# Kernel tuning notes

Hardware: AMD Instinct MI355X
Metric: run time of the kernel (lower is better)

The kernel has to match this reference:

```python
import jax, jax.numpy as jnp
import numpy as np


def setup_inputs() -> dict:
    key = jax.random.key(0)
    k1, k2 = jax.random.split(key)
    B, N, D = 16, 2048, 256      # batch, tokens, token_dim
    C, K = 8, 1024               # num_codebooks, num_tokens
    x_in = jax.random.normal(k1, (B, N, D), dtype=jnp.float32)
    # torch.rand init for each VQCodebook embedding -> uniform[0,1)
    codebooks = jax.random.uniform(k2, (C, K, D), dtype=jnp.float32)
    return {"x_in": x_in, "codebooks": codebooks}


def _apply_one_codebook(x_res, emb, code_sg):
    d2 = (
        jnp.sum(x_res * x_res, axis=-1, keepdims=True)
        - 2.0 * jnp.einsum("bnd,kd->bnk", x_res, emb)
        + jnp.sum(emb * emb, axis=-1)
    )
    idx = jnp.argmin(d2, axis=-1)          # (B,N)
    z_q = emb[idx]                         # (B,N,D) gather
    if code_sg:                            # straight-through estimator
        z_q = x_res + jax.lax.stop_gradient(z_q - x_res)
    return z_q, idx


def reference(x_in, codebooks, code_sg=True):
    C = codebooks.shape[0]
    x_res = x_in
    z_q = jnp.zeros_like(x_in)
    idx_list = []
    for i in range(C):  # sequential residual dependency, loop over fixed num_codebooks
        # faithful to original: subtracts CUMULATIVE z_q each iteration
        x_res = x_res - z_q
        z_q_i, idx_i = _apply_one_codebook(x_res, codebooks[i], code_sg)
        z_q = z_q + z_q_i
        idx_list.append(idx_i)
    indices = jnp.stack(idx_list, axis=-2)  # (B, C, N)
    return z_q, indices
```

## Files before the change

### kernel.cpp

```cpp
#include <hip/hip_runtime.h>

#define TOKENS   32768
#define DIM      256
#define KCB      1024
#define CBOOKS   8
#define NTOK     2048
#define ZQ_ELEMS (TOKENS * DIM)
#define EPS_GAP  2.0e-2f

typedef _Float16 f16x8 __attribute__((ext_vector_type(8)));
typedef float    f32x4 __attribute__((ext_vector_type(4)));

__device__ float np_pairwise_sumsq_256(const float4* a4) {
  #pragma clang fp contract(off)
  float h[2];
  for (int hh = 0; hh < 2; ++hh) {
    const float4* b = a4 + hh * 32;
    float4 v0 = b[0], v1 = b[1];
    float r0 = v0.x * v0.x, r1 = v0.y * v0.y, r2 = v0.z * v0.z, r3 = v0.w * v0.w;
    float r4 = v1.x * v1.x, r5 = v1.y * v1.y, r6 = v1.z * v1.z, r7 = v1.w * v1.w;
    for (int t = 1; t < 16; ++t) {
      float4 w0 = b[2 * t], w1 = b[2 * t + 1];
      r0 = r0 + w0.x * w0.x; r1 = r1 + w0.y * w0.y;
      r2 = r2 + w0.z * w0.z; r3 = r3 + w0.w * w0.w;
      r4 = r4 + w1.x * w1.x; r5 = r5 + w1.y * w1.y;
      r6 = r6 + w1.z * w1.z; r7 = r7 + w1.w * w1.w;
    }
    h[hh] = ((r0 + r1) + (r2 + r3)) + ((r4 + r5) + (r6 + r7));
  }
  return h[0] + h[1];
}

__device__ __forceinline__ float4 f4_muladd(float4 a, float4 b, float4 c) {
  #pragma clang fp contract(off)
  float4 r;
  r.x = a.x * b.x + c.x;
  r.y = a.y * b.y + c.y;
  r.z = a.z * b.z + c.z;
  r.w = a.w * b.w + c.w;
  return r;
}

__global__ __launch_bounds__(256) void rvq_norms_kernel(
    const float* __restrict__ cb, float* __restrict__ sume) {
  int row = blockIdx.x * 256 + threadIdx.x;
  sume[row] = np_pairwise_sumsq_256((const float4*)&cb[(size_t)row * DIM]);
}

__global__ __launch_bounds__(256) void rvq_efsplit_kernel(
    const float* __restrict__ cbc, f16x8* __restrict__ EfC) {
  int gw = blockIdx.x * 4 + (threadIdx.x >> 6);
  int l  = threadIdx.x & 63;
  int row = gw * 16 + (l & 15);
  #pragma unroll
  for (int kb = 0; kb < 8; ++kb) {
    int d0 = kb * 32 + ((l >> 4) << 3);
    float4 u = *(const float4*)&cbc[(size_t)row * DIM + d0];
    float4 v = *(const float4*)&cbc[(size_t)row * DIM + d0 + 4];
    float ev[8] = {u.x, u.y, u.z, u.w, v.x, v.y, v.z, v.w};
    f16x8 hi, lo;
    #pragma unroll
    for (int i = 0; i < 8; ++i) {
      _Float16 h = (_Float16)ev[i];
      hi[i] = h; lo[i] = (_Float16)(ev[i] - (float)h);
    }
    EfC[((size_t)gw * 16 + kb) * 64 + l]     = hi;
    EfC[((size_t)gw * 16 + kb + 8) * 64 + l] = lo;
  }
}

__global__ __launch_bounds__(256) void rvq_screen_kernel(
    const float* __restrict__ xr, const f16x8* __restrict__ EfC,
    const float* __restrict__ sume, float4* __restrict__ part,
    int* __restrict__ fix_cnt) {
  __shared__ f16x8 ldsA[2][8][64];

  const int tid  = threadIdx.x;
  const int lane = tid & 63;
  const int wid  = tid >> 6;
  const int wm   = wid & 1;
  const int wn   = wid >> 1;
  const int mtile = blockIdx.x & 255;
  const int ntile = blockIdx.x >> 8;
  const int m0  = mtile * 128;

  if (blockIdx.x == 0 && tid == 0) *fix_cnt = 0;

  const f16x8* EfW = EfC + ((size_t)(ntile * 8 + wn * 4) * 16) * 64 + lane;

  f32x4 acc[4][4];
  #pragma unroll
  for (int mi = 0; mi < 4; ++mi)
    #pragma unroll
    for (int ni = 0; ni < 4; ++ni) acc[mi][ni] = (f32x4){0.f, 0.f, 0.f, 0.f};

  float4 ga[2][2];

#define LOADG(KC_)                                                           \
  { _Pragma("unroll")                                                        \
    for (int j = 0; j < 2; ++j) {                                            \
      int item = j * 256 + tid;                                              \
      int row = item >> 2, q8 = item & 3;                                    \
      const float* sa = &xr[(size_t)(m0 + row) * DIM + (KC_) * 32 + q8 * 8]; \
      ga[j][0] = *(const float4*)sa; ga[j][1] = *(const float4*)(sa + 4);    \
    } }

#define CVW()                                                                \
  { _Pragma("unroll")                                                        \
    for (int j = 0; j < 2; ++j) {                                            \
      int item = j * 256 + tid;                                              \
      int row = item >> 2, q8 = item & 3;                                    \
      int fl = (row & 15) + 16 * q8, fr = row >> 4;                          \
      float4 u = ga[j][0], v = ga[j][1];                                     \
      float xv[8] = {u.x, u.y, u.z, u.w, v.x, v.y, v.z, v.w};                \
      f16x8 hi, lo;                                                          \
      _Pragma("unroll")                                                      \
      for (int i = 0; i < 8; ++i) {                                          \
        _Float16 h = (_Float16)xv[i];                                        \
        hi[i] = h; lo[i] = (_Float16)(xv[i] - (float)h);                     \
      }                                                                      \
      ldsA[0][fr][fl] = hi; ldsA[1][fr][fl] = lo;                            \
    } }

  LOADG(0)
  for (int kc = 0; kc < 8; ++kc) {
    f16x8 bh[4], bl[4];
    #pragma unroll
    for (int ni = 0; ni < 4; ++ni) {
      bh[ni] = EfW[(size_t)ni * 1024 + (size_t)kc * 64];
      bl[ni] = EfW[(size_t)ni * 1024 + (size_t)(kc + 8) * 64];
    }
    if (kc) __syncthreads();
    CVW()
    if (kc < 7) LOADG(kc + 1)
    __syncthreads();
    f16x8 ah[4], al[4];
    #pragma unroll
    for (int i = 0; i < 4; ++i) {
      ah[i] = ldsA[0][wm * 4 + i][lane];
      al[i] = ldsA[1][wm * 4 + i][lane];
    }
    #pragma unroll
    for (int mi = 0; mi < 4; ++mi)
      #pragma unroll
      for (int ni = 0; ni < 4; ++ni) {
        acc[mi][ni] = __builtin_amdgcn_mfma_f32_16x16x32_f16(
            ah[mi], bh[ni], acc[mi][ni], 0, 0, 0);
        acc[mi][ni] = __builtin_amdgcn_mfma_f32_16x16x32_f16(
            al[mi], bh[ni], acc[mi][ni], 0, 0, 0);
        acc[mi][ni] = __builtin_amdgcn_mfma_f32_16x16x32_f16(
            ah[mi], bl[ni], acc[mi][ni], 0, 0, 0);
      }
  }
#undef LOADG
#undef CVW
  __syncthreads();

  float* scr = (float*)&ldsA[0][0][0];
  const int n0 = ntile * 128 + wn * 64;
  float se[4];
  #pragma unroll
  for (int ni = 0; ni < 4; ++ni) se[ni] = sume[n0 + ni * 16 + (lane & 15)];

  #pragma unroll
  for (int mi = 0; mi < 4; ++mi) {
    #pragma unroll
    for (int r = 0; r < 4; ++r) {
      float v1 = 3.0e38f, v2 = 3.0e38f; int i1 = 0x7fffffff;
      #pragma unroll
      for (int ni = 0; ni < 4; ++ni) {
        float key = fmaf(-2.0f, acc[mi][ni][r], se[ni]);
        int   k   = n0 + ni * 16 + (lane & 15);
        if (key < v1 || (key == v1 && k < i1)) { v2 = v1; v1 = key; i1 = k; }
        else { v2 = fminf(v2, key); }
      }
      #pragma unroll
      for (int off = 1; off < 16; off <<= 1) {
        float ov1 = __shfl_xor(v1, off, 64);
        int   oi1 = __shfl_xor(i1, off, 64);
        float ov2 = __shfl_xor(v2, off, 64);
        if (ov1 < v1 || (ov1 == v1 && oi1 < i1)) { v2 = fminf(ov2, v1); v1 = ov1; i1 = oi1; }
        else { v2 = fminf(v2, fminf(ov1, ov2)); }
      }
      if ((lane & 15) == 0) {
        int tl = wm * 64 + mi * 16 + (lane >> 4) * 4 + r;
        scr[wn * 384 + tl]       = v1;
        scr[wn * 384 + 128 + tl] = __int_as_float(i1);
        scr[wn * 384 + 256 + tl] = v2;
      }
    }
  }
  __syncthreads();

  if (tid < 128) {
    float av1 = scr[tid],        av2 = scr[256 + tid];
    int   ai  = __float_as_int(scr[128 + tid]);
    float bv1 = scr[384 + tid],  bv2 = scr[384 + 256 + tid];
    int   bi  = __float_as_int(scr[384 + 128 + tid]);
    float v1, v2; int i1;
    if (bv1 < av1) { v1 = bv1; i1 = bi; v2 = fminf(bv2, av1); }
    else           { v1 = av1; i1 = ai; v2 = fminf(av2, bv1); }
    part[(size_t)ntile * TOKENS + m0 + tid] =
        make_float4(v1, __int_as_float(i1), v2, 0.0f);
  }
}

__global__ __launch_bounds__(256) void rvq_merge_kernel(
    const float4* __restrict__ part, int* __restrict__ idx_ws,
    int* __restrict__ fix_list, int* __restrict__ fix_cnt,
    float* __restrict__ idxf) {
  int token = blockIdx.x * 256 + threadIdx.x;
  float v1 = 3.0e38f, v2 = 3.0e38f; int i1 = 0x7fffffff;
  #pragma unroll
  for (int j = 0; j < 8; ++j) {
    float4 p = part[(size_t)j * TOKENS + token];
    float ov1 = p.x, ov2 = p.z; int oi1 = __float_as_int(p.y);
    if (ov1 < v1 || (ov1 == v1 && oi1 < i1)) { v2 = fminf(ov2, v1); v1 = ov1; i1 = oi1; }
    else { v2 = fminf(v2, fminf(ov1, ov2)); }
  }
  idx_ws[token] = i1;
  if (v2 - v1 < EPS_GAP) {
    int pos = atomicAdd(fix_cnt, 1);
    fix_list[pos] = token;
  }
  int b = token >> 11, n = token & (NTOK - 1);
  idxf[(size_t)b * (CBOOKS * NTOK) + n] = (float)i1;
}

__global__ __launch_bounds__(256, 2) void rvq_fixup_kernel(
    const float* __restrict__ xr, const float* __restrict__ cbc,
    const float* __restrict__ sume, const int* __restrict__ fix_list,
    const int* __restrict__ fix_cnt, int* __restrict__ idx_ws,
    float* __restrict__ idxf) {
  #pragma clang fp contract(off)
  __shared__ float xs[DIM];
  __shared__ float redv[4];
  __shared__ int   redi[4];
  __shared__ float sxv_sh;
  const int tid  = threadIdx.x;
  const int nfix = *fix_cnt;

  #pragma unroll 1
  for (int i = blockIdx.x; i < nfix; i += gridDim.x) {
    int token = fix_list[i];
    __syncthreads();
    if (tid < 64)
      ((float4*)xs)[tid] = ((const float4*)xr)[(size_t)token * 64 + tid];
    __syncthreads();
    if (tid < 64) {
      float s = 0.f;
      if ((tid & 63) < 16) {
        int j = tid & 7, hh = (tid >> 3) & 1;
        const float* bb = xs + hh * 128;
        float r = bb[j] * bb[j];
        #pragma unroll 1
        for (int t = 1; t < 16; ++t) r = r + bb[8 * t + j] * bb[8 * t + j];
        s = r;
      }
      #pragma unroll
      for (int off = 1; off <= 8; off <<= 1)
        s = s + __shfl_xor(s, off, 64);
      if (tid == 0) sxv_sh = s;
    }
    __syncthreads();
    float sxv = sxv_sh;
    float bv = 3.0e38f; int bi = 0x7fffffff;
    #pragma unroll 1
    for (int kk = 0; kk < 4; ++kk) {
      int k = kk * 256 + tid;
      float4 vacc = {0.f, 0.f, 0.f, 0.f};
      #pragma unroll 1
      for (int t = 0; t < 16; ++t) {
        float4 ab = vacc;
        #pragma unroll
        for (int j = 3; j >= 0; --j) {
          float4 xq = *(const float4*)&xs[t * 16 + j * 4];
          float4 eq = *(const float4*)&cbc[(size_t)k * DIM + t * 16 + j * 4];
          ab = f4_muladd(xq, eq, ab);
        }
        vacc = ab;
      }
      float dot = (vacc.x + vacc.y) + (vacc.z + vacc.w);
      float d2  = (sxv - 2.0f * dot) + sume[k];
      if (d2 < bv || (d2 == bv && k < bi)) { bv = d2; bi = k; }
    }
    #pragma unroll
    for (int off = 1; off < 64; off <<= 1) {
      float ov = __shfl_xor(bv, off, 64);
      int   oi = __shfl_xor(bi, off, 64);
      if (ov < bv || (ov == bv && oi < bi)) { bv = ov; bi = oi; }
    }
    int w = tid >> 6;
    if ((tid & 63) == 0) { redv[w] = bv; redi[w] = bi; }
    __syncthreads();
    if (tid == 0) {
      #pragma unroll
      for (int ww = 1; ww < 4; ++ww)
        if (redv[ww] < bv || (redv[ww] == bv && redi[ww] < bi)) { bv = redv[ww]; bi = redi[ww]; }
      idx_ws[token] = bi;
      int b = token >> 11, n = token & (NTOK - 1);
      idxf[(size_t)b * (CBOOKS * NTOK) + n] = (float)bi;
    }
  }
}

__global__ __launch_bounds__(256) void rvq_zq_resid_kernel(
    const float* __restrict__ xsrc, const float* __restrict__ cbc,
    const int* __restrict__ idx_ws, float* __restrict__ zq,
    float* __restrict__ xdst, int first, int last) {
  #pragma clang fp contract(off)
  int gid   = blockIdx.x * 256 + threadIdx.x;
  int token = gid >> 6;
  int q     = gid & 63;
  int idx   = idx_ws[token];
  float4 e = ((const float4*)cbc)[(size_t)idx * 64 + q];
  float4 x = ((const float4*)xsrc)[gid];
  float4 zi;
  zi.x = x.x + (e.x - x.x); zi.y = x.y + (e.y - x.y);
  zi.z = x.z + (e.z - x.z); zi.w = x.w + (e.w - x.w);
  float4 zo;
  if (first) { zo = zi; }
  else {
    float4 z = ((float4*)zq)[gid];
    zo.x = z.x + zi.x; zo.y = z.y + zi.y; zo.z = z.z + zi.z; zo.w = z.w + zi.w;
  }
  ((float4*)zq)[gid] = zo;
  if (!last) {
    float4 xn;
    xn.x = x.x - zo.x; xn.y = x.y - zo.y; xn.z = x.z - zo.z; xn.w = x.w - zo.w;
    ((float4*)xdst)[gid] = xn;
  }
}

extern "C" void kernel_launch(void* const* d_in, const int* in_sizes, int n_in,
                              void* d_out, int out_size, void* d_ws, size_t ws_size,
                              hipStream_t stream) {
  const float* x_in = (const float*)d_in[0];
  const float* cbs  = (const float*)d_in[1];
  float* zq      = (float*)d_out;
  float* idxbase = (float*)d_out + ZQ_ELEMS;

  char* ws = (char*)d_ws;
  float*  sume     = (float*)ws;
  int*    idx_ws   = (int*)(ws + (256 << 10));
  int*    fix_list = (int*)(ws + (448 << 10));
  int*    fix_cnt  = (int*)(ws + (640 << 10));
  float4* part     = (float4*)(ws + (1 << 20));
  f16x8*  EfC      = (f16x8*)(ws + (5 << 20));
  float*  xr       = (float*)(ws + (8 << 20));

  rvq_norms_kernel<<<32, 256, 0, stream>>>(cbs, sume);
  for (int c = 0; c < CBOOKS; ++c) {
    const float* src = (c == 0) ? x_in : xr;
    const float* cbc = cbs + (size_t)c * KCB * DIM;
    float* idxf = idxbase + (size_t)c * NTOK;
    rvq_efsplit_kernel<<<16, 256, 0, stream>>>(cbc, EfC);
    rvq_screen_kernel<<<2048, 256, 0, stream>>>(
        src, EfC, sume + (size_t)c * KCB, part, fix_cnt);
    rvq_merge_kernel<<<128, 256, 0, stream>>>(
        part, idx_ws, fix_list, fix_cnt, idxf);
    rvq_fixup_kernel<<<256, 256, 0, stream>>>(
        src, cbc, sume + (size_t)c * KCB, fix_list, fix_cnt, idx_ws, idxf);
    rvq_zq_resid_kernel<<<8192, 256, 0, stream>>>(
        src, cbc, idx_ws, zq, xr, c == 0, c == CBOOKS - 1);
  }
}
```

Measured before the change: 1.152 ms.

## Fuse screen and merge: keep A fragments in registers and loop over all codebook tiles

The screen kernel is restructured so each wave loads its 16 tokens once, splits them into fp16 hi/lo fragments held in registers, and then sweeps all 1024 codebook entries in 8 tiles. The B operand is double-buffered through LDS, and a running top-2 is kept per token. This removes the partial-result buffer and the separate merge kernel, and the fix_cnt reset moves into the efsplit kernel. In exchange the grid shrinks from 2048 to 512 blocks, register pressure rises, and every block now reads the whole split codebook.

```diff
diff --git a/kernel.cpp b/kernel.cpp
--- a/kernel.cpp
+++ b/kernel.cpp
@@ -48,7 +48,9 @@
 }
 
 __global__ __launch_bounds__(256) void rvq_efsplit_kernel(
-    const float* __restrict__ cbc, f16x8* __restrict__ EfC) {
+    const float* __restrict__ cbc, f16x8* __restrict__ EfC,
+    int* __restrict__ fix_cnt) {
+  if (blockIdx.x == 0 && threadIdx.x == 0) *fix_cnt = 0;
   int gw = blockIdx.x * 4 + (threadIdx.x >> 6);
   int l  = threadIdx.x & 63;
   int row = gw * 16 + (l & 15);
@@ -69,107 +71,84 @@
   }
 }
 
-__global__ __launch_bounds__(256) void rvq_screen_kernel(
+__global__ __launch_bounds__(256, 2) void rvq_screen_kernel(
     const float* __restrict__ xr, const f16x8* __restrict__ EfC,
-    const float* __restrict__ sume, float4* __restrict__ part,
-    int* __restrict__ fix_cnt) {
-  __shared__ f16x8 ldsA[2][8][64];
+    const float* __restrict__ sume, int* __restrict__ idx_ws,
+    int* __restrict__ fix_list, int* __restrict__ fix_cnt,
+    float* __restrict__ idxf) {
+  __shared__ f16x8 ldsB[2][8][2][64];
 
   const int tid  = threadIdx.x;
   const int lane = tid & 63;
-  const int wid  = tid >> 6;
-  const int wm   = wid & 1;
-  const int wn   = wid >> 1;
-  const int mtile = blockIdx.x & 255;
-  const int ntile = blockIdx.x >> 8;
-  const int m0  = mtile * 128;
-
-  if (blockIdx.x == 0 && tid == 0) *fix_cnt = 0;
-
-  const f16x8* EfW = EfC + ((size_t)(ntile * 8 + wn * 4) * 16) * 64 + lane;
-
-  f32x4 acc[4][4];
+  const int w    = tid >> 6;
+  const int m0w  = blockIdx.x * 64 + w * 16;
+
+  f16x8 ah[8], al[8];
+  {
+    const float* base = &xr[(size_t)(m0w + (lane & 15)) * DIM + ((lane >> 4) << 3)];
+    #pragma unroll
+    for (int kc = 0; kc < 8; ++kc) {
+      float4 u = *(const float4*)(base + kc * 32);
+      float4 v = *(const float4*)(base + kc * 32 + 4);
+      float xv[8] = {u.x, u.y, u.z, u.w, v.x, v.y, v.z, v.w};
+      #pragma unroll
+      for (int i = 0; i < 8; ++i) {
+        _Float16 h = (_Float16)xv[i];
+        ah[kc][i] = h; al[kc][i] = (_Float16)(xv[i] - (float)h);
+      }
+    }
+  }
+
+  float rv1[4], rv2[4]; int ri1[4];
   #pragma unroll
-  for (int mi = 0; mi < 4; ++mi)
-    #pragma unroll
-    for (int ni = 0; ni < 4; ++ni) acc[mi][ni] = (f32x4){0.f, 0.f, 0.f, 0.f};
-
-  float4 ga[2][2];
-
-#define LOADG(KC_)                                                           \
+  for (int r = 0; r < 4; ++r) { rv1[r] = 3.0e38f; rv2[r] = 3.0e38f; ri1[r] = 0x7fffffff; }
+
+#define STAGE_B(BUF, NT, KC)                                                 \
   { _Pragma("unroll")                                                        \
-    for (int j = 0; j < 2; ++j) {                                            \
-      int item = j * 256 + tid;                                              \
-      int row = item >> 2, q8 = item & 3;                                    \
-      const float* sa = &xr[(size_t)(m0 + row) * DIM + (KC_) * 32 + q8 * 8]; \
-      ga[j][0] = *(const float4*)sa; ga[j][1] = *(const float4*)(sa + 4);    \
+    for (int cc = 0; cc < 4; ++cc) {                                         \
+      int e = cc * 256 + tid;                                                \
+      int ln = e & 63, p = e >> 6;                          \
+      int ni = p >> 1, half = p & 1;                                         \
+      ldsB[BUF][ni][half][ln] =                                              \
+          EfC[(((size_t)(NT) * 8 + ni) * 16 + (half ? (KC) + 8 : (KC))) * 64 + ln]; \
     } }
 
-#define CVW()                                                                \
-  { _Pragma("unroll")                                                        \
-    for (int j = 0; j < 2; ++j) {                                            \
-      int item = j * 256 + tid;                                              \
-      int row = item >> 2, q8 = item & 3;                                    \
-      int fl = (row & 15) + 16 * q8, fr = row >> 4;                          \
-      float4 u = ga[j][0], v = ga[j][1];                                     \
-      float xv[8] = {u.x, u.y, u.z, u.w, v.x, v.y, v.z, v.w};                \
-      f16x8 hi, lo;                                                          \
-      _Pragma("unroll")                                                      \
-      for (int i = 0; i < 8; ++i) {                                          \
-        _Float16 h = (_Float16)xv[i];                                        \
-        hi[i] = h; lo[i] = (_Float16)(xv[i] - (float)h);                     \
-      }                                                                      \
-      ldsA[0][fr][fl] = hi; ldsA[1][fr][fl] = lo;                            \
-    } }
-
-  LOADG(0)
-  for (int kc = 0; kc < 8; ++kc) {
-    f16x8 bh[4], bl[4];
-    #pragma unroll
-    for (int ni = 0; ni < 4; ++ni) {
-      bh[ni] = EfW[(size_t)ni * 1024 + (size_t)kc * 64];
-      bl[ni] = EfW[(size_t)ni * 1024 + (size_t)(kc + 8) * 64];
-    }
-    if (kc) __syncthreads();
-    CVW()
-    if (kc < 7) LOADG(kc + 1)
-    __syncthreads();
-    f16x8 ah[4], al[4];
-    #pragma unroll
-    for (int i = 0; i < 4; ++i) {
-      ah[i] = ldsA[0][wm * 4 + i][lane];
-      al[i] = ldsA[1][wm * 4 + i][lane];
-    }
-    #pragma unroll
-    for (int mi = 0; mi < 4; ++mi)
-      #pragma unroll
-      for (int ni = 0; ni < 4; ++ni) {
-        acc[mi][ni] = __builtin_amdgcn_mfma_f32_16x16x32_f16(
-            ah[mi], bh[ni], acc[mi][ni], 0, 0, 0);
-        acc[mi][ni] = __builtin_amdgcn_mfma_f32_16x16x32_f16(
-            al[mi], bh[ni], acc[mi][ni], 0, 0, 0);
-        acc[mi][ni] = __builtin_amdgcn_mfma_f32_16x16x32_f16(
-            ah[mi], bl[ni], acc[mi][ni], 0, 0, 0);
-      }
-  }
-#undef LOADG
-#undef CVW
+  f32x4 acc[8];
+  #pragma unroll
+  for (int ni = 0; ni < 8; ++ni) acc[ni] = (f32x4){0.f, 0.f, 0.f, 0.f};
+
+  STAGE_B(0, 0, 0)
   __syncthreads();
 
-  float* scr = (float*)&ldsA[0][0][0];
-  const int n0 = ntile * 128 + wn * 64;
-  float se[4];
-  #pragma unroll
-  for (int ni = 0; ni < 4; ++ni) se[ni] = sume[n0 + ni * 16 + (lane & 15)];
-
-  #pragma unroll
-  for (int mi = 0; mi < 4; ++mi) {
+  #pragma unroll 1
+  for (int ntile = 0; ntile < 8; ++ntile) {
+    #pragma unroll
+    for (int kc = 0; kc < 8; ++kc) {
+      const int buf = kc & 1;
+      if (ntile * 8 + kc < 63) {
+        int nt2 = (kc < 7) ? ntile : ntile + 1;
+        STAGE_B(buf ^ 1, nt2, (kc + 1) & 7)
+      }
+      #pragma unroll
+      for (int ni = 0; ni < 8; ++ni) {
+        f16x8 bh = ldsB[buf][ni][0][lane];
+        f16x8 bl = ldsB[buf][ni][1][lane];
+        acc[ni] = __builtin_amdgcn_mfma_f32_16x16x32_f16(ah[kc], bh, acc[ni], 0, 0, 0);
+        acc[ni] = __builtin_amdgcn_mfma_f32_16x16x32_f16(al[kc], bh, acc[ni], 0, 0, 0);
+        acc[ni] = __builtin_amdgcn_mfma_f32_16x16x32_f16(ah[kc], bl, acc[ni], 0, 0, 0);
+      }
+      __syncthreads();
+    }
+    const int n0 = ntile * 128;
+    float se[8];
+    #pragma unroll
+    for (int ni = 0; ni < 8; ++ni) se[ni] = sume[n0 + ni * 16 + (lane & 15)];
     #pragma unroll
     for (int r = 0; r < 4; ++r) {
       float v1 = 3.0e38f, v2 = 3.0e38f; int i1 = 0x7fffffff;
       #pragma unroll
-      for (int ni = 0; ni < 4; ++ni) {
-        float key = fmaf(-2.0f, acc[mi][ni][r], se[ni]);
+      for (int ni = 0; ni < 8; ++ni) {
+        float key = fmaf(-2.0f, acc[ni][r], se[ni]);
         int   k   = n0 + ni * 16 + (lane & 15);
         if (key < v1 || (key == v1 && k < i1)) { v2 = v1; v1 = key; i1 = k; }
         else { v2 = fminf(v2, key); }
@@ -182,49 +161,28 @@
         if (ov1 < v1 || (ov1 == v1 && oi1 < i1)) { v2 = fminf(ov2, v1); v1 = ov1; i1 = oi1; }
         else { v2 = fminf(v2, fminf(ov1, ov2)); }
       }
-      if ((lane & 15) == 0) {
-        int tl = wm * 64 + mi * 16 + (lane >> 4) * 4 + r;
-        scr[wn * 384 + tl]       = v1;
-        scr[wn * 384 + 128 + tl] = __int_as_float(i1);
-        scr[wn * 384 + 256 + tl] = v2;
-      }
-    }
-  }
-  __syncthreads();
-
-  if (tid < 128) {
-    float av1 = scr[tid],        av2 = scr[256 + tid];
-    int   ai  = __float_as_int(scr[128 + tid]);
-    float bv1 = scr[384 + tid],  bv2 = scr[384 + 256 + tid];
-    int   bi  = __float_as_int(scr[384 + 128 + tid]);
-    float v1, v2; int i1;
-    if (bv1 < av1) { v1 = bv1; i1 = bi; v2 = fminf(bv2, av1); }
-    else           { v1 = av1; i1 = ai; v2 = fminf(av2, bv1); }
-    part[(size_t)ntile * TOKENS + m0 + tid] =
-        make_float4(v1, __int_as_float(i1), v2, 0.0f);
-  }
-}
-
-__global__ __launch_bounds__(256) void rvq_merge_kernel(
-    const float4* __restrict__ part, int* __restrict__ idx_ws,
-    int* __restrict__ fix_list, int* __restrict__ fix_cnt,
-    float* __restrict__ idxf) {
-  int token = blockIdx.x * 256 + threadIdx.x;
-  float v1 = 3.0e38f, v2 = 3.0e38f; int i1 = 0x7fffffff;
-  #pragma unroll
-  for (int j = 0; j < 8; ++j) {
-    float4 p = part[(size_t)j * TOKENS + token];
-    float ov1 = p.x, ov2 = p.z; int oi1 = __float_as_int(p.y);
-    if (ov1 < v1 || (ov1 == v1 && oi1 < i1)) { v2 = fminf(ov2, v1); v1 = ov1; i1 = oi1; }
-    else { v2 = fminf(v2, fminf(ov1, ov2)); }
-  }
-  idx_ws[token] = i1;
-  if (v2 - v1 < EPS_GAP) {
-    int pos = atomicAdd(fix_cnt, 1);
-    fix_list[pos] = token;
-  }
-  int b = token >> 11, n = token & (NTOK - 1);
-  idxf[(size_t)b * (CBOOKS * NTOK) + n] = (float)i1;
+      if (v1 < rv1[r] || (v1 == rv1[r] && i1 < ri1[r])) {
+        rv2[r] = fminf(rv1[r], v2); rv1[r] = v1; ri1[r] = i1;
+      } else { rv2[r] = fminf(rv2[r], fminf(v1, v2)); }
+    }
+    #pragma unroll
+    for (int ni = 0; ni < 8; ++ni) acc[ni] = (f32x4){0.f, 0.f, 0.f, 0.f};
+  }
+#undef STAGE_B
+
+  if ((lane & 15) == 0) {
+    #pragma unroll
+    for (int r = 0; r < 4; ++r) {
+      int token = m0w + (lane >> 4) * 4 + r;
+      idx_ws[token] = ri1[r];
+      if (rv2[r] - rv1[r] < EPS_GAP) {
+        int pos = atomicAdd(fix_cnt, 1);
+        fix_list[pos] = token;
+      }
+      int b = token >> 11, n = token & (NTOK - 1);
+      idxf[(size_t)b * (CBOOKS * NTOK) + n] = (float)ri1[r];
+    }
+  }
 }
 
 __global__ __launch_bounds__(256, 2) void rvq_fixup_kernel(
@@ -345,7 +303,6 @@
   int*    idx_ws   = (int*)(ws + (256 << 10));
   int*    fix_list = (int*)(ws + (448 << 10));
   int*    fix_cnt  = (int*)(ws + (640 << 10));
-  float4* part     = (float4*)(ws + (1 << 20));
   f16x8*  EfC      = (f16x8*)(ws + (5 << 20));
   float*  xr       = (float*)(ws + (8 << 20));
 
@@ -354,11 +311,9 @@
     const float* src = (c == 0) ? x_in : xr;
     const float* cbc = cbs + (size_t)c * KCB * DIM;
     float* idxf = idxbase + (size_t)c * NTOK;
-    rvq_efsplit_kernel<<<16, 256, 0, stream>>>(cbc, EfC);
-    rvq_screen_kernel<<<2048, 256, 0, stream>>>(
-        src, EfC, sume + (size_t)c * KCB, part, fix_cnt);
-    rvq_merge_kernel<<<128, 256, 0, stream>>>(
-        part, idx_ws, fix_list, fix_cnt, idxf);
+    rvq_efsplit_kernel<<<16, 256, 0, stream>>>(cbc, EfC, fix_cnt);
+    rvq_screen_kernel<<<512, 256, 0, stream>>>(
+        src, EfC, sume + (size_t)c * KCB, idx_ws, fix_list, fix_cnt, idxf);
     rvq_fixup_kernel<<<256, 256, 0, stream>>>(
         src, cbc, sume + (size_t)c * KCB, fix_list, fix_cnt, idx_ws, idxf);
     rvq_zq_resid_kernel<<<8192, 256, 0, stream>>>(
```

Result: faster. 1.114 ms (-3.3%).
